# Optimization experiments

Hardware: AMD Instinct MI355X
Metric: run time of the kernel (lower is better)

## Reference

```python
import jax, jax.numpy as jnp
import numpy as np

NEG_SLOPE = 0.2


def add_self_loops(edge_index, num_nodes):
    loop = jnp.arange(num_nodes, dtype=edge_index.dtype)
    return jnp.concatenate([edge_index, jnp.stack([loop, loop])], axis=1)


def gat_conv(x, edge_index, W, att_src, att_dst, bias, heads, out_ch, concat):
    # x: [N, F_in]; edge_index: [2, E]; W: [F_in, heads*out_ch]
    # att_src/att_dst: [heads, out_ch]; bias: [heads*out_ch] or [out_ch]
    N = x.shape[0]
    ei = add_self_loops(edge_index, N)
    src, dst = ei[0], ei[1]
    xw = (x @ W).reshape(N, heads, out_ch)          # [N, H, C]
    a_src = jnp.einsum('nhc,hc->nh', xw, att_src)    # [N, H]
    a_dst = jnp.einsum('nhc,hc->nh', xw, att_dst)    # [N, H]
    e = a_src[src] + a_dst[dst]                      # [E', H]
    e = jax.nn.leaky_relu(e, NEG_SLOPE)
    # segment softmax over edges grouped by destination node
    e_max = jax.ops.segment_max(e, dst, num_segments=N)  # [N, H]
    e_exp = jnp.exp(e - e_max[dst])
    denom = jax.ops.segment_sum(e_exp, dst, num_segments=N)  # [N, H]
    alpha = e_exp / denom[dst]                       # [E', H]
    msg = xw[src] * alpha[:, :, None]                # [E', H, C]
    out = jax.ops.segment_sum(msg, dst, num_segments=N)  # [N, H, C]
    if concat:
        out = out.reshape(N, heads * out_ch)
    else:
        out = out.mean(axis=1)
    return out + bias


def setup_inputs() -> dict:
    key = jax.random.key(0)
    ks = jax.random.split(key, 10)
    N, E = 100000, 1600000
    F_in, hid, heads, F_out = 128, 32, 4, 40
    s = 0.1
    x = jax.random.normal(ks[0], (N, F_in), dtype=jnp.float32)
    edge_index = jax.random.randint(ks[1], (2, E), 0, N, dtype=jnp.int64)
    W1 = jax.random.normal(ks[2], (F_in, heads * hid), dtype=jnp.float32) * s
    att_src1 = jax.random.normal(ks[3], (heads, hid), dtype=jnp.float32) * s
    att_dst1 = jax.random.normal(ks[4], (heads, hid), dtype=jnp.float32) * s
    b1 = jax.random.normal(ks[5], (heads * hid,), dtype=jnp.float32) * s
    W2 = jax.random.normal(ks[6], (heads * hid, F_out), dtype=jnp.float32) * s
    att_src2 = jax.random.normal(ks[7], (1, F_out), dtype=jnp.float32) * s
    att_dst2 = jax.random.normal(ks[8], (1, F_out), dtype=jnp.float32) * s
    b2 = jax.random.normal(ks[9], (F_out,), dtype=jnp.float32) * s
    return {"x": x, "edge_index": edge_index, "W1": W1, "att_src1": att_src1,
            "att_dst1": att_dst1, "b1": b1, "W2": W2, "att_src2": att_src2,
            "att_dst2": att_dst2, "b2": b2}


def reference(x, edge_index, W1, att_src1, att_dst1, b1, W2, att_src2, att_dst2, b2):
    h = gat_conv(x, edge_index, W1, att_src1, att_dst1, b1, heads=4, out_ch=32, concat=True)
    h = jax.nn.relu(h)
    out = gat_conv(h, edge_index, W2, att_src2, att_dst2, b2, heads=1, out_ch=40, concat=True)
    return out
```

## Files before the change

kernel.cpp:

```cpp
#include <hip/hip_runtime.h>
#include <hip/hip_bf16.h>

#define NEG_SLOPE 0.2f
#define LOG2E 1.4426950408889634f
#define HWREG_XCC_ID_FULL (((32 - 1) << 11) | (0 << 6) | 20)

typedef _Float16 f16;
typedef f16 f16x8 __attribute__((ext_vector_type(8)));
typedef float f32x4 __attribute__((ext_vector_type(4)));

__device__ __forceinline__ unsigned pack_h2(float a, float b) {
    union { f16 h[2]; unsigned u; } c;
    c.h[0] = (f16)a; c.h[1] = (f16)b;
    return c.u;
}

__global__ void k_detect(const int* __restrict__ ei32, int npairs, int* flag) {
    __shared__ int found;
    if (threadIdx.x == 0) found = 0;
    __syncthreads();
    for (int i = threadIdx.x; i < npairs; i += blockDim.x) {
        if (ei32[2 * i + 1] != 0) found = 1;
    }
    __syncthreads();
    if (threadIdx.x == 0) *flag = found ? 0 : 1;
}

__device__ __forceinline__ void load_edge(const void* ei, int f64, int e, int E, int& s, int& d) {
    if (f64) {
        const long long* p = (const long long*)ei;
        s = (int)p[e];
        d = (int)p[(long long)E + e];
    } else {
        const int* p = (const int*)ei;
        s = p[e];
        d = p[E + e];
    }
}

__global__ void k_degree(const void* __restrict__ ei, const int* __restrict__ flag,
                         int* __restrict__ deg_part, int* __restrict__ rank, int N, int E) {
    int e = blockIdx.x * blockDim.x + threadIdx.x;
    if (e >= E) return;
    int s, d;
    load_edge(ei, *flag, e, E, s, d);
    int xcc = (int)(__builtin_amdgcn_s_getreg(HWREG_XCC_ID_FULL) & 7u);
    int lr = atomicAdd(&deg_part[xcc * N + d], 1);
    rank[e] = (xcc << 24) | lr;
}

__global__ void k_sumdeg(int* __restrict__ deg_part, int* __restrict__ deg, int N) {
    int d = blockIdx.x * blockDim.x + threadIdx.x;
    if (d >= N) return;
    int p = 0;
#pragma unroll
    for (int x = 0; x < 8; x++) {
        int t = deg_part[x * N + d];
        deg_part[x * N + d] = p;
        p += t;
    }
    deg[d] = p;
}

__global__ __launch_bounds__(1024) void k_scan_blk(const int* __restrict__ deg,
                                                   int* __restrict__ offsets,
                                                   int* __restrict__ blksum, int N) {
    __shared__ int wsums[16];
    const int t = threadIdx.x;
    const int lane = t & 63;
    const int wid = t >> 6;
    int idx = blockIdx.x * 4096 + t * 4;
    int v0 = (idx + 0 < N) ? deg[idx + 0] : 0;
    int v1 = (idx + 1 < N) ? deg[idx + 1] : 0;
    int v2 = (idx + 2 < N) ? deg[idx + 2] : 0;
    int v3 = (idx + 3 < N) ? deg[idx + 3] : 0;
    int s1 = v0 + v1, s2 = s1 + v2, s3 = s2 + v3;
    int inc = s3;
#pragma unroll
    for (int off = 1; off < 64; off <<= 1) {
        int y = __shfl_up(inc, off);
        if (lane >= off) inc += y;
    }
    if (lane == 63) wsums[wid] = inc;
    __syncthreads();
    if (wid == 0) {
        int v = (lane < 16) ? wsums[lane] : 0;
        int wi = v;
#pragma unroll
        for (int off = 1; off < 16; off <<= 1) {
            int y = __shfl_up(wi, off);
            if (lane >= off) wi += y;
        }
        if (lane < 16) wsums[lane] = wi - v;
        if (lane == 15) blksum[blockIdx.x] = wi;
    }
    __syncthreads();
    int excl = wsums[wid] + (inc - s3);
    if (idx + 0 < N) offsets[idx + 1] = excl + v0;
    if (idx + 1 < N) offsets[idx + 2] = excl + s1;
    if (idx + 2 < N) offsets[idx + 3] = excl + s2;
    if (idx + 3 < N) offsets[idx + 4] = excl + s3;
}

__global__ void k_scan_top(const int* __restrict__ blksum, int* __restrict__ blkoff, int G) {
    int l = threadIdx.x;
    int v = (l < G) ? blksum[l] : 0;
    int inc = v;
#pragma unroll
    for (int off = 1; off < 64; off <<= 1) {
        int y = __shfl_up(inc, off);
        if (l >= off) inc += y;
    }
    if (l < G) blkoff[l] = inc - v;
}

__global__ void k_scan_add(int* __restrict__ offsets, const int* __restrict__ blkoff, int N) {
    int n = blockIdx.x * blockDim.x + threadIdx.x;
    if (n >= N) return;
    offsets[n + 1] += blkoff[n >> 12];
    if (n == 0) offsets[0] = 0;
}

__global__ void k_scatter(const void* __restrict__ ei, const int* __restrict__ flag,
                          const int* __restrict__ offsets, const int* __restrict__ deg_part,
                          const int* __restrict__ rank, int* __restrict__ csr_src,
                          int N, int E) {
    int e = blockIdx.x * blockDim.x + threadIdx.x;
    if (e >= E) return;
    int s, d;
    load_edge(ei, *flag, e, E, s, d);
    int r = rank[e];
    int xcc = r >> 24;
    int lr = r & 0xFFFFFF;
    csr_src[offsets[d] + deg_part[xcc * N + d] + lr] = s;
}

__global__ void k_prep(const float* __restrict__ W1, const float* __restrict__ W2,
                       f16* __restrict__ W1t, f16* __restrict__ W2t) {
    int o = blockIdx.x * 256 + threadIdx.x;
    if (o < 128 * 128) {
        int n = o >> 7, k = o & 127;
        W1t[o] = (f16)W1[k * 128 + n];
    } else {
        int o2 = o - 128 * 128;
        if (o2 < 48 * 128) {
            int n = o2 >> 7, k = o2 & 127;
            W2t[o2] = (f16)(n < 40 ? W2[k * 40 + n] : 0.f);
        }
    }
}

__global__ __launch_bounds__(256) void k_gemm1(const float* __restrict__ X,
                                               const f16* __restrict__ W1t,
                                               const float* __restrict__ as1,
                                               const float* __restrict__ ad1,
                                               f16* __restrict__ Af,
                                               float* __restrict__ aS1,
                                               float* __restrict__ aD1, int N) {
    __shared__ f16 sA[64 * 136];
    __shared__ f16 sB[128 * 136];
    const int t = threadIdx.x;
    const int row0 = blockIdx.x * 64;

    {
        int r = t >> 2, seg = t & 3;
        int row = row0 + r;
        if (row >= N) row = N - 1;
        const float4* xg = (const float4*)(X + (size_t)row * 128 + seg * 32);
        unsigned tmp[16];
#pragma unroll
        for (int j = 0; j < 8; j++) {
            float4 v = xg[j];
            tmp[2 * j]     = pack_h2(v.x, v.y);
            tmp[2 * j + 1] = pack_h2(v.z, v.w);
        }
        uint4* dst = (uint4*)&sA[r * 136 + seg * 32];
#pragma unroll
        for (int j = 0; j < 4; j++) dst[j] = ((uint4*)tmp)[j];
        int n = t >> 1, half = (t & 1) * 64;
        const uint4* src = (const uint4*)(W1t + n * 128 + half);
        uint4* dw = (uint4*)&sB[n * 136 + half];
#pragma unroll
        for (int j = 0; j < 8; j++) dw[j] = src[j];
    }
    __syncthreads();

    const int w = t >> 6, lane = t & 63, ln = lane & 15, q = lane >> 4;
    f32x4 acc[8];
#pragma unroll
    for (int c = 0; c < 8; c++) acc[c] = (f32x4){0.f, 0.f, 0.f, 0.f};

#pragma unroll
    for (int ks = 0; ks < 4; ks++) {
        f16x8 a = *(const f16x8*)&sA[(w * 16 + ln) * 136 + ks * 32 + q * 8];
#pragma unroll
        for (int c = 0; c < 8; c++) {
            f16x8 b = *(const f16x8*)&sB[(c * 16 + ln) * 136 + ks * 32 + q * 8];
            acc[c] = __builtin_amdgcn_mfma_f32_16x16x32_f16(a, b, acc[c], 0, 0, 0);
        }
    }

#pragma unroll
    for (int c = 0; c < 8; c++)
#pragma unroll
        for (int reg = 0; reg < 4; reg++) {
            int rg = row0 + w * 16 + q * 4 + reg;
            if (rg < N) Af[(size_t)rg * 128 + c * 16 + ln] = (f16)acc[c][reg];
        }

    float ps[4][4], pd[4][4];
#pragma unroll
    for (int h = 0; h < 4; h++) {
        float as_lo = as1[32 * h + ln], as_hi = as1[32 * h + 16 + ln];
        float ad_lo = ad1[32 * h + ln], ad_hi = ad1[32 * h + 16 + ln];
#pragma unroll
        for (int reg = 0; reg < 4; reg++) {
            ps[h][reg] = acc[2 * h][reg] * as_lo + acc[2 * h + 1][reg] * as_hi;
            pd[h][reg] = acc[2 * h][reg] * ad_lo + acc[2 * h + 1][reg] * ad_hi;
        }
    }
#pragma unroll
    for (int h = 0; h < 4; h++)
#pragma unroll
        for (int reg = 0; reg < 4; reg++)
#pragma unroll
            for (int off = 1; off < 16; off <<= 1) {
                ps[h][reg] += __shfl_xor(ps[h][reg], off);
                pd[h][reg] += __shfl_xor(pd[h][reg], off);
            }
#pragma unroll
    for (int h = 0; h < 4; h++) {
        if (ln == 2 * h) {
#pragma unroll
            for (int reg = 0; reg < 4; reg++) {
                int rg = row0 + w * 16 + q * 4 + reg;
                if (rg < N) aS1[rg * 4 + h] = ps[h][reg] * LOG2E;
            }
        }
        if (ln == 2 * h + 1) {
#pragma unroll
            for (int reg = 0; reg < 4; reg++) {
                int rg = row0 + w * 16 + q * 4 + reg;
                if (rg < N) aD1[rg * 4 + h] = pd[h][reg] * LOG2E;
            }
        }
    }
}

__global__ __launch_bounds__(256) void k_gemm2(const f16* __restrict__ Hf,
                                               const f16* __restrict__ W2t,
                                               const float* __restrict__ as2,
                                               const float* __restrict__ ad2,
                                               f16* __restrict__ X2f,
                                               float* __restrict__ aS2,
                                               float* __restrict__ aD2, int N) {
    __shared__ f16 sA[64 * 136];
    __shared__ f16 sB[48 * 136];
    const int t = threadIdx.x;
    const int row0 = blockIdx.x * 64;
    {
        int r = t >> 2, seg = t & 3;
        int row = row0 + r;
        if (row >= N) row = N - 1;
        const uint4* hg = (const uint4*)(Hf + (size_t)row * 128 + seg * 32);
        uint4* dst = (uint4*)&sA[r * 136 + seg * 32];
#pragma unroll
        for (int j = 0; j < 4; j++) dst[j] = hg[j];
        const uint4* wsrc = (const uint4*)W2t;
#pragma unroll
        for (int u = t; u < 768; u += 256) {
            int o = u * 8;
            int n = o >> 7, ko = o & 127;
            *(uint4*)&sB[n * 136 + ko] = wsrc[u];
        }
    }
    __syncthreads();

    const int w = t >> 6, lane = t & 63, ln = lane & 15, q = lane >> 4;
    f32x4 acc[3];
#pragma unroll
    for (int c = 0; c < 3; c++) acc[c] = (f32x4){0.f, 0.f, 0.f, 0.f};

#pragma unroll
    for (int ks = 0; ks < 4; ks++) {
        f16x8 a = *(const f16x8*)&sA[(w * 16 + ln) * 136 + ks * 32 + q * 8];
#pragma unroll
        for (int c = 0; c < 3; c++) {
            f16x8 b = *(const f16x8*)&sB[(c * 16 + ln) * 136 + ks * 32 + q * 8];
            acc[c] = __builtin_amdgcn_mfma_f32_16x16x32_f16(a, b, acc[c], 0, 0, 0);
        }
    }

#pragma unroll
    for (int c = 0; c < 3; c++) {
        int col = c * 16 + ln;
        if (col < 40) {
#pragma unroll
            for (int reg = 0; reg < 4; reg++) {
                int rg = row0 + w * 16 + q * 4 + reg;
                if (rg < N) X2f[(size_t)rg * 64 + col] = (f16)acc[c][reg];
            }
        }
    }

    float ps[4], pd[4];
#pragma unroll
    for (int reg = 0; reg < 4; reg++) { ps[reg] = 0.f; pd[reg] = 0.f; }
#pragma unroll
    for (int c = 0; c < 3; c++) {
        int col = c * 16 + ln;
        float as_ = (col < 40) ? as2[col] : 0.f;
        float ad_ = (col < 40) ? ad2[col] : 0.f;
#pragma unroll
        for (int reg = 0; reg < 4; reg++) {
            ps[reg] = fmaf(acc[c][reg], as_, ps[reg]);
            pd[reg] = fmaf(acc[c][reg], ad_, pd[reg]);
        }
    }
#pragma unroll
    for (int reg = 0; reg < 4; reg++) {
#pragma unroll
        for (int off = 1; off < 16; off <<= 1) {
            ps[reg] += __shfl_xor(ps[reg], off);
            pd[reg] += __shfl_xor(pd[reg], off);
        }
        int rg = row0 + w * 16 + q * 4 + reg;
        if (rg < N) {
            if (ln == 0) aS2[rg] = ps[reg] * LOG2E;
            if (ln == 1) aD2[rg] = pd[reg] * LOG2E;
        }
    }
}

__global__ __launch_bounds__(128) void k_msg1(const int* __restrict__ offsets,
                                              const int* __restrict__ csr_src,
                                              const float* __restrict__ aS,
                                              const float* __restrict__ aD,
                                              const f16* __restrict__ Af,
                                              const float* __restrict__ b1,
                                              f16* __restrict__ Hf, int N) {
    const int lane = threadIdx.x & 63;
    const int n = blockIdx.x * 2 + (threadIdx.x >> 6);
    const bool node_ok = (n < N);
    const int g = lane >> 4;
    const int p = lane & 15;
    const int h = p >> 2;

    int b = 0, e = 0;
    float adh = 0.f;
    if (node_ok) {
        b = offsets[n];
        e = offsets[n + 1];
        adh = aD[n * 4 + h];
    }

    float acc[8];
#pragma unroll
    for (int k = 0; k < 8; k++) acc[k] = 0.f;
    float wsum = 0.f;

    if (node_ok) {
        float xs = aS[n * 4 + h] + adh;
        float ws = __builtin_amdgcn_exp2f(fmaxf(xs, NEG_SLOPE * xs));
        if (g != 0) ws = 0.f;
        const f16x8 hv = *(const f16x8*)(Af + (size_t)n * 128 + p * 8);
#pragma unroll
        for (int k = 0; k < 8; k++) acc[k] = fmaf(ws, (float)hv[k], acc[k]);
        wsum = ws;
    }

    int sreg = 0;
    if (node_ok && e > b) {
        int idx = b + lane;
        if (idx >= e) idx = e - 1;
        sreg = csr_src[idx];
    }

    int i = b;
#pragma unroll 4
    for (; i < e && (i - b) + 4 <= 64; i += 4) {
        int j = i + g;
        bool valid = (j < e);
        int s = __builtin_amdgcn_ds_bpermute((j - b) << 2, sreg);
        if (!valid) s = 0;
        float sv = aS[s * 4 + h];
        const f16x8 hv = *(const f16x8*)(Af + (size_t)s * 128 + p * 8);
        float x = sv + adh;
        float wgt = __builtin_amdgcn_exp2f(fmaxf(x, NEG_SLOPE * x));
        if (!valid) wgt = 0.f;
#pragma unroll
        for (int k = 0; k < 8; k++) acc[k] = fmaf(wgt, (float)hv[k], acc[k]);
        wsum += wgt;
    }
    for (; i < e; i += 4) {
        int j = i + g;
        bool valid = (j < e);
        int jc = valid ? j : (e - 1);
        int s = csr_src[jc];
        if (!valid) s = 0;
        float sv = aS[s * 4 + h];
        const f16x8 hv = *(const f16x8*)(Af + (size_t)s * 128 + p * 8);
        float x = sv + adh;
        float wgt = __builtin_amdgcn_exp2f(fmaxf(x, NEG_SLOPE * x));
        if (!valid) wgt = 0.f;
#pragma unroll
        for (int k = 0; k < 8; k++) acc[k] = fmaf(wgt, (float)hv[k], acc[k]);
        wsum += wgt;
    }

#pragma unroll
    for (int k = 0; k < 8; k++) {
        acc[k] += __shfl_xor(acc[k], 16);
        acc[k] += __shfl_xor(acc[k], 32);
    }
    wsum += __shfl_xor(wsum, 16);
    wsum += __shfl_xor(wsum, 32);

    if (node_ok && g == 0) {
        float inv = __builtin_amdgcn_rcpf(wsum);
        const float4* bb = (const float4*)(b1 + p * 8);
        float4 b0 = bb[0], b4 = bb[1];
        float bv[8] = {b0.x, b0.y, b0.z, b0.w, b4.x, b4.y, b4.z, b4.w};
        union { f16 h8[8]; uint4 u; } o;
#pragma unroll
        for (int k = 0; k < 8; k++) {
            float v = fmaf(acc[k], inv, bv[k]);
            o.h8[k] = (f16)fmaxf(v, 0.f);
        }
        *(uint4*)(Hf + (size_t)n * 128 + p * 8) = o.u;
    }
}

__global__ __launch_bounds__(128) void k_msg2(const int* __restrict__ offsets,
                                              const int* __restrict__ csr_src,
                                              const float* __restrict__ aS,
                                              const float* __restrict__ aD,
                                              const f16* __restrict__ X2f,
                                              const float* __restrict__ b2,
                                              float* __restrict__ OUT, int N) {
    __shared__ float red[2][60][9];
    const int lane = threadIdx.x & 63;
    const int wv = threadIdx.x >> 6;
    const int n = blockIdx.x * 2 + wv;
    const bool node_ok = (n < N);
    const int g = lane / 5;
    const int p = lane % 5;
    const bool lane_ok = (g < 12);

    int b = 0, e = 0;
    float adh = 0.f;
    if (node_ok) {
        b = offsets[n];
        e = offsets[n + 1];
        adh = aD[n];
    }

    float acc[8];
#pragma unroll
    for (int k = 0; k < 8; k++) acc[k] = 0.f;
    float wsum = 0.f;

    if (node_ok) {
        float xs = aS[n] + adh;
        float ws = __builtin_amdgcn_exp2f(fmaxf(xs, NEG_SLOPE * xs));
        if (!(lane_ok && g == 0)) ws = 0.f;
        const f16x8 hv = *(const f16x8*)(X2f + (size_t)n * 64 + p * 8);
#pragma unroll
        for (int k = 0; k < 8; k++) acc[k] = fmaf(ws, (float)hv[k], acc[k]);
        wsum = ws;
    }

    int sreg = 0;
    if (node_ok && e > b) {
        int idx = b + lane;
        if (idx >= e) idx = e - 1;
        sreg = csr_src[idx];
    }

    int i = b;
    for (; i < e && (i - b) + 12 <= 64; i += 12) {
        int j = i + g;
        bool valid = lane_ok && (j < e);
        int s = __builtin_amdgcn_ds_bpermute(((j - b) & 63) << 2, sreg);
        if (!valid) s = 0;
        float sv = aS[s];
        const f16x8 hv = *(const f16x8*)(X2f + (size_t)s * 64 + p * 8);
        float x = sv + adh;
        float wgt = __builtin_amdgcn_exp2f(fmaxf(x, NEG_SLOPE * x));
        if (!valid) wgt = 0.f;
#pragma unroll
        for (int k = 0; k < 8; k++) acc[k] = fmaf(wgt, (float)hv[k], acc[k]);
        wsum += wgt;
    }
    for (; i < e; i += 12) {
        int j = i + g;
        bool valid = lane_ok && (j < e);
        int jc = (j < e) ? j : (e - 1);
        int s = csr_src[jc];
        if (!valid) s = 0;
        float sv = aS[s];
        const f16x8 hv = *(const f16x8*)(X2f + (size_t)s * 64 + p * 8);
        float x = sv + adh;
        float wgt = __builtin_amdgcn_exp2f(fmaxf(x, NEG_SLOPE * x));
        if (!valid) wgt = 0.f;
#pragma unroll
        for (int k = 0; k < 8; k++) acc[k] = fmaf(wgt, (float)hv[k], acc[k]);
        wsum += wgt;
    }

    if (lane_ok) {
#pragma unroll
        for (int k = 0; k < 8; k++) red[wv][lane][k] = acc[k];
        red[wv][lane][8] = wsum;
    }
    __syncthreads();

    if (node_ok && lane < 40) {
        int pp = lane >> 3, kk = lane & 7;
        float s_ = 0.f, ws_ = 0.f;
#pragma unroll
        for (int gg = 0; gg < 12; gg++) {
            s_  += red[wv][gg * 5 + pp][kk];
            ws_ += red[wv][gg * 5][8];
        }
        float inv = __builtin_amdgcn_rcpf(ws_);
        OUT[(size_t)n * 40 + lane] = fmaf(s_, inv, b2[lane]);
    }
}

extern "C" void kernel_launch(void* const* d_in, const int* in_sizes, int n_in,
                              void* d_out, int out_size, void* d_ws, size_t ws_size,
                              hipStream_t stream) {
    const float* x   = (const float*)d_in[0];
    const void*  ei  = d_in[1];
    const float* W1  = (const float*)d_in[2];
    const float* as1 = (const float*)d_in[3];
    const float* ad1 = (const float*)d_in[4];
    const float* b1  = (const float*)d_in[5];
    const float* W2  = (const float*)d_in[6];
    const float* as2 = (const float*)d_in[7];
    const float* ad2 = (const float*)d_in[8];
    const float* b2  = (const float*)d_in[9];
    float* out = (float*)d_out;

    const int N = in_sizes[0] / 128;
    const int E = in_sizes[1] / 2;

    char* w = (char*)d_ws;
    auto alloc = [&](size_t bytes) {
        char* p = w;
        w += (bytes + 15) & ~(size_t)15;
        return p;
    };
    int* flag      = (int*)alloc(16);
    int* offsets   = (int*)alloc((size_t)(N + 1) * 4);
    int* deg       = (int*)alloc((size_t)N * 4);
    int* deg_part  = (int*)alloc((size_t)N * 8 * 4);
    int* rank      = (int*)alloc((size_t)E * 4);
    int* csr_src   = (int*)alloc((size_t)E * 4);
    int* blksum    = (int*)alloc(64 * 4);
    int* blkoff    = (int*)alloc(64 * 4);
    float* aS1     = (float*)alloc((size_t)N * 4 * 4);
    float* aD1     = (float*)alloc((size_t)N * 4 * 4);
    float* aS2     = (float*)alloc((size_t)N * 4);
    float* aD2     = (float*)alloc((size_t)N * 4);
    f16* W1t       = (f16*)alloc(128 * 128 * 2);
    f16* W2t       = (f16*)alloc(48 * 128 * 2);
    f16* Af        = (f16*)alloc((size_t)N * 128 * 2);
    f16* X2f       = (f16*)alloc((size_t)N * 64 * 2);
    f16* Hf        = (f16*)alloc((size_t)N * 128 * 2);

    k_detect<<<1, 256, 0, stream>>>((const int*)ei, 1024, flag);
    k_prep<<<88, 256, 0, stream>>>(W1, W2, W1t, W2t);

    hipMemsetAsync(deg_part, 0, (size_t)N * 8 * 4, stream);
    k_degree<<<(E + 255) / 256, 256, 0, stream>>>(ei, flag, deg_part, rank, N, E);
    k_sumdeg<<<(N + 255) / 256, 256, 0, stream>>>(deg_part, deg, N);
    const int G = (N + 4095) / 4096;
    k_scan_blk<<<G, 1024, 0, stream>>>(deg, offsets, blksum, N);
    k_scan_top<<<1, 64, 0, stream>>>(blksum, blkoff, G);
    k_scan_add<<<(N + 255) / 256, 256, 0, stream>>>(offsets, blkoff, N);
    k_scatter<<<(E + 255) / 256, 256, 0, stream>>>(ei, flag, offsets, deg_part, rank,
                                                   csr_src, N, E);

    const int gb = (N + 63) / 64;
    k_gemm1<<<gb, 256, 0, stream>>>(x, W1t, as1, ad1, Af, aS1, aD1, N);
    k_msg1<<<(N + 1) / 2, 128, 0, stream>>>(offsets, csr_src, aS1, aD1, Af, b1, Hf, N);

    k_gemm2<<<gb, 256, 0, stream>>>(Hf, W2t, as2, ad2, X2f, aS2, aD2, N);
    k_msg2<<<(N + 1) / 2, 128, 0, stream>>>(offsets, csr_src, aS2, aD2, X2f, b2, out, N);
}
```

Measured before the change: 388.3 us.

## Split layer-1 features into head-pair halves and run message pass in two passes

Stores the layer-1 projected features and hidden output as two half-width planes (heads 0-1 and heads 2-3). The first message kernel now runs two passes over all nodes, each gathering only 64-wide rows, so each pass has a smaller working set that fits better in cache, and each wave handles 8 edges at a time. It also merges the detect, weight-prep and memset launches into a single init kernel, and folds the per-XCC degree prefix into the block scan so the sumdeg kernel goes away. The cost is a second pass that re-reads the CSR and attention scores, plus added shuffle reductions.

```diff
diff --git a/kernel.cpp b/kernel.cpp
--- a/kernel.cpp
+++ b/kernel.cpp
@@ -13,17 +13,6 @@
     union { f16 h[2]; unsigned u; } c;
     c.h[0] = (f16)a; c.h[1] = (f16)b;
     return c.u;
-}
-
-__global__ void k_detect(const int* __restrict__ ei32, int npairs, int* flag) {
-    __shared__ int found;
-    if (threadIdx.x == 0) found = 0;
-    __syncthreads();
-    for (int i = threadIdx.x; i < npairs; i += blockDim.x) {
-        if (ei32[2 * i + 1] != 0) found = 1;
-    }
-    __syncthreads();
-    if (threadIdx.x == 0) *flag = found ? 0 : 1;
 }
 
 __device__ __forceinline__ void load_edge(const void* ei, int f64, int e, int E, int& s, int& d) {
@@ -38,31 +27,51 @@
     }
 }
 
+__global__ void k_init(const int* __restrict__ ei32, int npairs, int* __restrict__ flag,
+                       const float* __restrict__ W1, const float* __restrict__ W2,
+                       f16* __restrict__ W1t, f16* __restrict__ W2t,
+                       uint4* __restrict__ deg_part4, int nzero) {
+    const int b = blockIdx.x, t = threadIdx.x;
+    if (b == 0) {
+        __shared__ int found;
+        if (t == 0) found = 0;
+        __syncthreads();
+        for (int i = t; i < npairs; i += 256) {
+            if (ei32[2 * i + 1] != 0) found = 1;
+        }
+        __syncthreads();
+        if (t == 0) *flag = found ? 0 : 1;
+    } else if (b <= 88) {
+        int o = (b - 1) * 256 + t;
+        if (o < 128 * 128) {
+            int n = o >> 7, k = o & 127;
+            W1t[o] = (f16)W1[k * 128 + n];
+        } else {
+            int o2 = o - 128 * 128;
+            if (o2 < 48 * 128) {
+                int n = o2 >> 7, k = o2 & 127;
+                W2t[o2] = (f16)(n < 40 ? W2[k * 40 + n] : 0.f);
+            }
+        }
+    } else {
+        int idx = (b - 89) * 256 + t;
+        if (idx < nzero) deg_part4[idx] = (uint4){0, 0, 0, 0};
+    }
+}
+
 __global__ void k_degree(const void* __restrict__ ei, const int* __restrict__ flag,
                          int* __restrict__ deg_part, int* __restrict__ rank, int N, int E) {
     int e = blockIdx.x * blockDim.x + threadIdx.x;
     if (e >= E) return;
-    int s, d;
-    load_edge(ei, *flag, e, E, s, d);
+    int d;
+    if (*flag) d = (int)((const long long*)ei)[(long long)E + e];
+    else       d = ((const int*)ei)[E + e];
     int xcc = (int)(__builtin_amdgcn_s_getreg(HWREG_XCC_ID_FULL) & 7u);
     int lr = atomicAdd(&deg_part[xcc * N + d], 1);
     rank[e] = (xcc << 24) | lr;
 }
 
-__global__ void k_sumdeg(int* __restrict__ deg_part, int* __restrict__ deg, int N) {
-    int d = blockIdx.x * blockDim.x + threadIdx.x;
-    if (d >= N) return;
-    int p = 0;
-#pragma unroll
-    for (int x = 0; x < 8; x++) {
-        int t = deg_part[x * N + d];
-        deg_part[x * N + d] = p;
-        p += t;
-    }
-    deg[d] = p;
-}
-
-__global__ __launch_bounds__(1024) void k_scan_blk(const int* __restrict__ deg,
+__global__ __launch_bounds__(1024) void k_scan_blk(int* __restrict__ deg_part,
                                                    int* __restrict__ offsets,
                                                    int* __restrict__ blksum, int N) {
     __shared__ int wsums[16];
@@ -70,10 +79,37 @@
     const int lane = t & 63;
     const int wid = t >> 6;
     int idx = blockIdx.x * 4096 + t * 4;
-    int v0 = (idx + 0 < N) ? deg[idx + 0] : 0;
-    int v1 = (idx + 1 < N) ? deg[idx + 1] : 0;
-    int v2 = (idx + 2 < N) ? deg[idx + 2] : 0;
-    int v3 = (idx + 3 < N) ? deg[idx + 3] : 0;
+    int v0 = 0, v1 = 0, v2 = 0, v3 = 0;
+    if (((N & 3) == 0) && (idx + 3 < N)) {
+        uint4 u[8];
+#pragma unroll
+        for (int x = 0; x < 8; x++) u[x] = *(uint4*)&deg_part[x * N + idx];
+        int p0 = 0, p1 = 0, p2 = 0, p3 = 0;
+#pragma unroll
+        for (int x = 0; x < 8; x++) {
+            uint4 w = u[x];
+            u[x] = (uint4){(unsigned)p0, (unsigned)p1, (unsigned)p2, (unsigned)p3};
+            p0 += (int)w.x; p1 += (int)w.y; p2 += (int)w.z; p3 += (int)w.w;
+        }
+#pragma unroll
+        for (int x = 0; x < 8; x++) *(uint4*)&deg_part[x * N + idx] = u[x];
+        v0 = p0; v1 = p1; v2 = p2; v3 = p3;
+    } else if (idx < N) {
+        int vv[4] = {0, 0, 0, 0};
+        for (int i = 0; i < 4; i++) {
+            int d = idx + i;
+            if (d >= N) break;
+            int p = 0;
+#pragma unroll
+            for (int x = 0; x < 8; x++) {
+                int t0 = deg_part[x * N + d];
+                deg_part[x * N + d] = p;
+                p += t0;
+            }
+            vv[i] = p;
+        }
+        v0 = vv[0]; v1 = vv[1]; v2 = vv[2]; v3 = vv[3];
+    }
     int s1 = v0 + v1, s2 = s1 + v2, s3 = s2 + v3;
     int inc = s3;
 #pragma unroll
@@ -135,26 +171,11 @@
     csr_src[offsets[d] + deg_part[xcc * N + d] + lr] = s;
 }
 
-__global__ void k_prep(const float* __restrict__ W1, const float* __restrict__ W2,
-                       f16* __restrict__ W1t, f16* __restrict__ W2t) {
-    int o = blockIdx.x * 256 + threadIdx.x;
-    if (o < 128 * 128) {
-        int n = o >> 7, k = o & 127;
-        W1t[o] = (f16)W1[k * 128 + n];
-    } else {
-        int o2 = o - 128 * 128;
-        if (o2 < 48 * 128) {
-            int n = o2 >> 7, k = o2 & 127;
-            W2t[o2] = (f16)(n < 40 ? W2[k * 40 + n] : 0.f);
-        }
-    }
-}
-
 __global__ __launch_bounds__(256) void k_gemm1(const float* __restrict__ X,
                                                const f16* __restrict__ W1t,
                                                const float* __restrict__ as1,
                                                const float* __restrict__ ad1,
-                                               f16* __restrict__ Af,
+                                               f16* __restrict__ Afh,
                                                float* __restrict__ aS1,
                                                float* __restrict__ aD1, int N) {
     __shared__ f16 sA[64 * 136];
@@ -200,13 +221,16 @@
         }
     }
 
-#pragma unroll
-    for (int c = 0; c < 8; c++)
+    const size_t H64 = (size_t)N * 64;
+#pragma unroll
+    for (int c = 0; c < 8; c++) {
+        int half = c >> 2, cc = c & 3;
 #pragma unroll
         for (int reg = 0; reg < 4; reg++) {
             int rg = row0 + w * 16 + q * 4 + reg;
-            if (rg < N) Af[(size_t)rg * 128 + c * 16 + ln] = (f16)acc[c][reg];
-        }
+            if (rg < N) Afh[half * H64 + (size_t)rg * 64 + cc * 16 + ln] = (f16)acc[c][reg];
+        }
+    }
 
     float ps[4][4], pd[4][4];
 #pragma unroll
@@ -247,7 +271,7 @@
     }
 }
 
-__global__ __launch_bounds__(256) void k_gemm2(const f16* __restrict__ Hf,
+__global__ __launch_bounds__(256) void k_gemm2(const f16* __restrict__ Hfh,
                                                const f16* __restrict__ W2t,
                                                const float* __restrict__ as2,
                                                const float* __restrict__ ad2,
@@ -258,11 +282,13 @@
     __shared__ f16 sB[48 * 136];
     const int t = threadIdx.x;
     const int row0 = blockIdx.x * 64;
+    const size_t H64 = (size_t)N * 64;
     {
         int r = t >> 2, seg = t & 3;
         int row = row0 + r;
         if (row >= N) row = N - 1;
-        const uint4* hg = (const uint4*)(Hf + (size_t)row * 128 + seg * 32);
+        const uint4* hg = (const uint4*)(Hfh + (size_t)(seg >> 1) * H64 +
+                                         (size_t)row * 64 + (seg & 1) * 32);
         uint4* dst = (uint4*)&sA[r * 136 + seg * 32];
 #pragma unroll
         for (int j = 0; j < 4; j++) dst[j] = hg[j];
@@ -336,15 +362,19 @@
                                               const int* __restrict__ csr_src,
                                               const float* __restrict__ aS,
                                               const float* __restrict__ aD,
-                                              const f16* __restrict__ Af,
+                                              const f16* __restrict__ Afh,
                                               const float* __restrict__ b1,
-                                              f16* __restrict__ Hf, int N) {
+                                              f16* __restrict__ Hfh, int N, int NB) {
     const int lane = threadIdx.x & 63;
-    const int n = blockIdx.x * 2 + (threadIdx.x >> 6);
+    const int pass = (blockIdx.x >= NB) ? 1 : 0;
+    const int blk = blockIdx.x - pass * NB;
+    const int n = blk * 2 + (threadIdx.x >> 6);
     const bool node_ok = (n < N);
-    const int g = lane >> 4;
-    const int p = lane & 15;
-    const int h = p >> 2;
+    const int g = lane >> 3;
+    const int p = lane & 7;
+    const int h = pass * 2 + (p >> 2);
+    const size_t H64 = (size_t)N * 64;
+    const f16* Af = Afh + (size_t)pass * H64;
 
     int b = 0, e = 0;
     float adh = 0.f;
@@ -363,7 +393,7 @@
         float xs = aS[n * 4 + h] + adh;
         float ws = __builtin_amdgcn_exp2f(fmaxf(xs, NEG_SLOPE * xs));
         if (g != 0) ws = 0.f;
-        const f16x8 hv = *(const f16x8*)(Af + (size_t)n * 128 + p * 8);
+        const f16x8 hv = *(const f16x8*)(Af + (size_t)n * 64 + p * 8);
 #pragma unroll
         for (int k = 0; k < 8; k++) acc[k] = fmaf(ws, (float)hv[k], acc[k]);
         wsum = ws;
@@ -377,14 +407,14 @@
     }
 
     int i = b;
-#pragma unroll 4
-    for (; i < e && (i - b) + 4 <= 64; i += 4) {
+#pragma unroll 2
+    for (; i < e && (i - b) + 8 <= 64; i += 8) {
         int j = i + g;
         bool valid = (j < e);
         int s = __builtin_amdgcn_ds_bpermute((j - b) << 2, sreg);
         if (!valid) s = 0;
         float sv = aS[s * 4 + h];
-        const f16x8 hv = *(const f16x8*)(Af + (size_t)s * 128 + p * 8);
+        const f16x8 hv = *(const f16x8*)(Af + (size_t)s * 64 + p * 8);
         float x = sv + adh;
         float wgt = __builtin_amdgcn_exp2f(fmaxf(x, NEG_SLOPE * x));
         if (!valid) wgt = 0.f;
@@ -392,14 +422,14 @@
         for (int k = 0; k < 8; k++) acc[k] = fmaf(wgt, (float)hv[k], acc[k]);
         wsum += wgt;
     }
-    for (; i < e; i += 4) {
+    for (; i < e; i += 8) {
         int j = i + g;
         bool valid = (j < e);
         int jc = valid ? j : (e - 1);
         int s = csr_src[jc];
         if (!valid) s = 0;
         float sv = aS[s * 4 + h];
-        const f16x8 hv = *(const f16x8*)(Af + (size_t)s * 128 + p * 8);
+        const f16x8 hv = *(const f16x8*)(Af + (size_t)s * 64 + p * 8);
         float x = sv + adh;
         float wgt = __builtin_amdgcn_exp2f(fmaxf(x, NEG_SLOPE * x));
         if (!valid) wgt = 0.f;
@@ -410,15 +440,17 @@
 
 #pragma unroll
     for (int k = 0; k < 8; k++) {
+        acc[k] += __shfl_xor(acc[k], 8);
         acc[k] += __shfl_xor(acc[k], 16);
         acc[k] += __shfl_xor(acc[k], 32);
     }
+    wsum += __shfl_xor(wsum, 8);
     wsum += __shfl_xor(wsum, 16);
     wsum += __shfl_xor(wsum, 32);
 
     if (node_ok && g == 0) {
         float inv = __builtin_amdgcn_rcpf(wsum);
-        const float4* bb = (const float4*)(b1 + p * 8);
+        const float4* bb = (const float4*)(b1 + pass * 64 + p * 8);
         float4 b0 = bb[0], b4 = bb[1];
         float bv[8] = {b0.x, b0.y, b0.z, b0.w, b4.x, b4.y, b4.z, b4.w};
         union { f16 h8[8]; uint4 u; } o;
@@ -427,7 +459,7 @@
             float v = fmaf(acc[k], inv, bv[k]);
             o.h8[k] = (f16)fmaxf(v, 0.f);
         }
-        *(uint4*)(Hf + (size_t)n * 128 + p * 8) = o.u;
+        *(uint4*)(Hfh + (size_t)pass * H64 + (size_t)n * 64 + p * 8) = o.u;
     }
 }
 
@@ -554,7 +586,6 @@
     };
     int* flag      = (int*)alloc(16);
     int* offsets   = (int*)alloc((size_t)(N + 1) * 4);
-    int* deg       = (int*)alloc((size_t)N * 4);
     int* deg_part  = (int*)alloc((size_t)N * 8 * 4);
     int* rank      = (int*)alloc((size_t)E * 4);
     int* csr_src   = (int*)alloc((size_t)E * 4);
@@ -566,27 +597,27 @@
     float* aD2     = (float*)alloc((size_t)N * 4);
     f16* W1t       = (f16*)alloc(128 * 128 * 2);
     f16* W2t       = (f16*)alloc(48 * 128 * 2);
-    f16* Af        = (f16*)alloc((size_t)N * 128 * 2);
+    f16* Afh       = (f16*)alloc((size_t)N * 128 * 2);
     f16* X2f       = (f16*)alloc((size_t)N * 64 * 2);
-    f16* Hf        = (f16*)alloc((size_t)N * 128 * 2);
-
-    k_detect<<<1, 256, 0, stream>>>((const int*)ei, 1024, flag);
-    k_prep<<<88, 256, 0, stream>>>(W1, W2, W1t, W2t);
-
-    hipMemsetAsync(deg_part, 0, (size_t)N * 8 * 4, stream);
+    f16* Hfh       = (f16*)alloc((size_t)N * 128 * 2);
+
+    const int nzero = 2 * N;
+    k_init<<<89 + (nzero + 255) / 256, 256, 0, stream>>>(
+        (const int*)ei, 1024, flag, W1, W2, W1t, W2t, (uint4*)deg_part, nzero);
+
     k_degree<<<(E + 255) / 256, 256, 0, stream>>>(ei, flag, deg_part, rank, N, E);
-    k_sumdeg<<<(N + 255) / 256, 256, 0, stream>>>(deg_part, deg, N);
     const int G = (N + 4095) / 4096;
-    k_scan_blk<<<G, 1024, 0, stream>>>(deg, offsets, blksum, N);
+    k_scan_blk<<<G, 1024, 0, stream>>>(deg_part, offsets, blksum, N);
     k_scan_top<<<1, 64, 0, stream>>>(blksum, blkoff, G);
     k_scan_add<<<(N + 255) / 256, 256, 0, stream>>>(offsets, blkoff, N);
     k_scatter<<<(E + 255) / 256, 256, 0, stream>>>(ei, flag, offsets, deg_part, rank,
                                                    csr_src, N, E);
 
     const int gb = (N + 63) / 64;
-    k_gemm1<<<gb, 256, 0, stream>>>(x, W1t, as1, ad1, Af, aS1, aD1, N);
-    k_msg1<<<(N + 1) / 2, 128, 0, stream>>>(offsets, csr_src, aS1, aD1, Af, b1, Hf, N);
-
-    k_gemm2<<<gb, 256, 0, stream>>>(Hf, W2t, as2, ad2, X2f, aS2, aD2, N);
+    k_gemm1<<<gb, 256, 0, stream>>>(x, W1t, as1, ad1, Afh, aS1, aD1, N);
+    const int NB = (N + 1) / 2;
+    k_msg1<<<2 * NB, 128, 0, stream>>>(offsets, csr_src, aS1, aD1, Afh, b1, Hfh, N, NB);
+
+    k_gemm2<<<gb, 256, 0, stream>>>(Hfh, W2t, as2, ad2, X2f, aS2, aD2, N);
     k_msg2<<<(N + 1) / 2, 128, 0, stream>>>(offsets, csr_src, aS2, aD2, X2f, b2, out, N);
 }
```

Result: slower. 405.3 us (+4.4%).
